# Optimization experiments

Hardware: AMD Instinct MI355X
Metric: run time of the kernel (lower is better)

## Reference

```python
import jax, jax.numpy as jnp
import numpy as np
import math

H, N2, RANK, CH, LMAX = 256, 64, 1, 1, 2048
DT_MIN, DT_MAX = 1e-3, 1e-1


def setup_inputs() -> dict:
    key = jax.random.key(0)
    kP, kPi, kC, kCi, kdt = jax.random.split(key, 5)
    # DPLR 'lin' init: A = -1/2 - i*pi*n  (real_part=0.5, imag_part=pi*arange(N//2))
    A_real = 0.5 * jnp.ones((H, N2), jnp.float32)
    A_imag = math.pi * jnp.broadcast_to(jnp.arange(N2, dtype=jnp.float32), (H, N2))
    # B_init='constant': B = ones (complex)
    B_real = jnp.ones((H, N2), jnp.float32)
    B_imag = jnp.zeros((H, N2), jnp.float32)
    # P = randn complex (rank, H, N//2); torch complex randn has per-component std 1/sqrt(2)
    s = 1.0 / math.sqrt(2.0)
    P_real = s * jax.random.normal(kP, (RANK, H, N2), jnp.float32)
    P_imag = s * jax.random.normal(kPi, (RANK, H, N2), jnp.float32)
    # C (output projection) randn complex (channels, H, N//2)
    C_real = s * jax.random.normal(kC, (CH, H, N2), jnp.float32)
    C_imag = s * jax.random.normal(kCi, (CH, H, N2), jnp.float32)
    # dt log-uniform in [dt_min, dt_max]
    log_dt = math.log(DT_MIN) + jax.random.uniform(kdt, (H,), jnp.float32) * (
        math.log(DT_MAX) - math.log(DT_MIN))
    return {
        "A_real": A_real, "A_imag": A_imag,
        "B_real": B_real, "B_imag": B_imag,
        "P_real": P_real, "P_imag": P_imag,
        "C_real": C_real, "C_imag": C_imag,
        "log_dt": log_dt, "L": LMAX,
    }


def _krylov_doubling(dA, dB, L):
    """Matrix-power doubling scan (mirrors `power`): columns [dB, dA dB, ..., dA^{L-1} dB].

    dA: (H, N, N) complex, dB: (H, N) complex -> (H, N, L) complex.
    """
    x = dB[..., None]  # (H, N, 1)
    Ap = dA
    while x.shape[-1] < L:
        x = jnp.concatenate([x, Ap @ x], axis=-1)  # doubling step
        Ap = Ap @ Ap  # repeated squaring, as in power()
    return x[..., :L]


def reference(A_real, A_imag, B_real, B_imag, P_real, P_imag, C_real, C_imag, log_dt, L):
    # Build DPLR state matrix: A = diag(Lambda) - P P^*
    Lam = (-A_real - 1j * A_imag).astype(jnp.complex64)        # (H, N2)
    P = (P_real + 1j * P_imag).astype(jnp.complex64)           # (R, H, N2)
    B = (B_real + 1j * B_imag).astype(jnp.complex64)           # (H, N2)
    C = (C_real + 1j * C_imag).astype(jnp.complex64)           # (CH, H, N2)
    n2 = Lam.shape[-1]
    I = jnp.eye(n2, dtype=jnp.complex64)
    A_mat = Lam[:, :, None] * I - jnp.einsum('rhn,rhm->hnm', P, jnp.conj(P))  # (H,N2,N2)
    dt = jnp.exp(log_dt).astype(jnp.complex64)                 # (H,)
    # Bilinear (Tustin) discretization: dA = (I - dt/2 A)^{-1}(I + dt/2 A), dB = (I - dt/2 A)^{-1} dt B
    half = 0.5 * dt[:, None, None] * A_mat
    M_bwd = I - half
    dA = jnp.linalg.solve(M_bwd, I + half)                     # (H,N2,N2)
    dB = jnp.linalg.solve(M_bwd, (dt[:, None] * B)[..., None])[..., 0]  # (H,N2)
    # Kernel via power-doubling Krylov scan, then project: K[c,h,l] = 2 Re(C dA^l dB)
    x = _krylov_doubling(dA, dB, L)                            # (H,N2,L)
    K = 2.0 * jnp.real(jnp.einsum('chn,hnl->chl', C, x))       # (CH,H,L)
    return K
```

## Files before the change

### kernel.cpp

```cpp
#include <hip/hip_runtime.h>


#define LL 2048

struct C2 { float re, im; };

__device__ __forceinline__ C2 cmul(C2 a, C2 b){ return {a.re*b.re - a.im*b.im, a.re*b.im + a.im*b.re}; }
__device__ __forceinline__ C2 cadd(C2 a, C2 b){ return {a.re+b.re, a.im+b.im}; }
__device__ __forceinline__ C2 csub(C2 a, C2 b){ return {a.re-b.re, a.im-b.im}; }
__device__ __forceinline__ C2 cinv(C2 a){ float s=1.0f/(a.re*a.re+a.im*a.im); return {a.re*s, -a.im*s}; }
__device__ __forceinline__ C2 cscale(float s, C2 a){ return {s*a.re, s*a.im}; }
__device__ __forceinline__ C2 ld2(float2 v){ return {v.x, v.y}; }
__device__ __forceinline__ float2 st2(C2 v){ return make_float2(v.re, v.im); }

template<int CTRL>
__device__ __forceinline__ float dpp_add(float x){
  int t = __builtin_amdgcn_update_dpp(0, __float_as_int(x), CTRL, 0xF, 0xF, true);
  return x + __int_as_float(t);
}
__device__ __forceinline__ float wave_sum63(float x){
  x = dpp_add<0xB1>(x);
  x = dpp_add<0x4E>(x);
  x = dpp_add<0x124>(x);
  x = dpp_add<0x128>(x);
  x = dpp_add<0x142>(x);
  x = dpp_add<0x143>(x);
  return x;
}
__device__ __forceinline__ float bcast63(float x){
  return __int_as_float(__builtin_amdgcn_readlane(__float_as_int(x), 63));
}
__device__ __forceinline__ float rdlane(float v, int l){
  return __int_as_float(__builtin_amdgcn_readlane(__float_as_int(v), l));
}
__device__ __forceinline__ float shr1(float x){
  return __int_as_float(__builtin_amdgcn_update_dpp(0, __float_as_int(x), 0x138, 0xF, 0xF, true));
}

__device__ __forceinline__ void tri_solve64(const C2 wl, C2 va, const int lane,
                                            float& so_re, float& so_im)
{
    C2 wsh = { shr1(wl.re), shr1(wl.im) };
    const float w0r = rdlane(wl.re, 0);
    const float w0i = rdlane(wl.im, 0);
    so_re = 0.0f; so_im = 0.0f;
    for (int j = 0; j < 64; j += 2) {
        const float s0r = rdlane(va.re, j);
        const float s0i = rdlane(va.im, j);
        const float v1r = rdlane(va.re, j + 1);
        const float v1i = rdlane(va.im, j + 1);
        const float s1r = v1r + (w0r*s0r - w0i*s0i);
        const float s1i = v1i + (w0r*s0i + w0i*s0r);
        if (lane == j)     { so_re = s0r; so_im = s0i; }
        if (lane == j + 1) { so_re = s1r; so_im = s1i; }
        const C2 wsh1 = { shr1(wsh.re), shr1(wsh.im) };
        va.re += wsh.re*s0r - wsh.im*s0i;
        va.im += wsh.re*s0i + wsh.im*s0r;
        va.re += wsh1.re*s1r - wsh1.im*s1i;
        va.im += wsh1.re*s1i + wsh1.im*s1r;
        wsh.re = shr1(wsh1.re);
        wsh.im = shr1(wsh1.im);
    }
}

__global__ __launch_bounds__(512)
__attribute__((amdgpu_waves_per_eu(2, 2)))
void ssm_dplr_kernel(
    const float* __restrict__ A_real, const float* __restrict__ A_imag,
    const float* __restrict__ B_real, const float* __restrict__ B_imag,
    const float* __restrict__ P_real, const float* __restrict__ P_imag,
    const float* __restrict__ C_real, const float* __restrict__ C_imag,
    const float* __restrict__ log_dt, float* __restrict__ out)
{
    const int h    = blockIdx.x;
    const int t    = threadIdx.x;
    const int lane = t & 63;
    const int wid  = t >> 6;

    extern __shared__ char sm[];
    float2* Abuf = (float2*)sm;
    float2* Cs   = (float2*)(sm + 32768);
    float2* tw   = Cs;
    float2* ta   = Cs + 512;
    float2* gA   = (float2*)(sm + 49152);
    float2* qA   = gA + 64;
    float2* g64A = gA + 128;
    float2* TgA  = gA + 192;
    float2* TpA  = gA + 256;
    float2* rqA  = gA + 320;
    float2* rxA  = gA + 384;
    float2* wvA  = gA + 448;
    float2* avA  = gA + 512;
    float2* cbuf = gA + 576;
    float2* prtC = gA + 640;
    int*    cntA = (int*)(gA + 1152);
    int*    flgA = cntA + 32;

    const int idx = h * 64 + lane;
    const float dt = expf(log_dt[h]);
    const float c  = 0.5f * dt;

    const C2 lam = { -A_real[idx], -A_imag[idx] };
    const C2 p   = {  P_real[idx],  P_imag[idx] };
    const C2 Bv  = {  B_real[idx],  B_imag[idx] };
    const C2 Cv  = {  C_real[idx],  C_imag[idx] };
    const C2 pc  = { p.re, -p.im };

    const C2 d = cinv(C2{ 1.0f - c*lam.re, -c*lam.im });
    const C2 g = cmul(d, C2{ 1.0f + c*lam.re, c*lam.im });

    C2 sv = cscale(p.re*p.re + p.im*p.im, d);
    C2 uv = cmul(cmul(d, pc), Bv);
    sv.re = bcast63(wave_sum63(sv.re)); sv.im = bcast63(wave_sum63(sv.im));
    uv.re = bcast63(wave_sum63(uv.re)); uv.im = bcast63(wave_sum63(uv.im));

    const C2 beta  = cscale(c, cinv(C2{ 1.0f + c*sv.re, c*sv.im }));
    const C2 bs    = cmul(beta, sv);
    const C2 gamma = { -c*(1.0f - bs.re), c*bs.im };

    const C2 q  = cmul(d, p);
    const C2 r  = cmul(pc, csub(gamma, cmul(beta, g)));
    const C2 x0 = cscale(dt, csub(cmul(d, Bv), cmul(cmul(beta, uv), q)));

    const C2 g2  = cmul(g,  g);
    const C2 g4  = cmul(g2, g2);
    const C2 g8  = cmul(g4, g4);
    const C2 g16 = cmul(g8, g8);
    const C2 g32 = cmul(g16,g16);
    const C2 g64 = cmul(g32,g32);

    if (wid == 0) {
        gA[lane]   = st2(g);
        qA[lane]   = st2(q);
        g64A[lane] = st2(g64);
        rqA[lane]  = st2(cmul(r, q));
        rxA[lane]  = st2(cmul(r, x0));
    }
    __syncthreads();

    {
        C2 cur = {1.0f, 0.0f};
        if (wid & 1) cur = g8;
        if (wid & 2) cur = cmul(cur, g16);
        if (wid & 4) cur = cmul(cur, g32);
        #pragma unroll
        for (int jj = 0; jj < 8; ++jj) {
            const int j = 8*wid + jj;
            Abuf[j*64 + ((lane + j) & 63)] = st2(cur);
            cur = cmul(cur, g);
        }
    }
    __syncthreads();

    {
        C2 accw = {0,0}, acca = {0,0};
        #pragma unroll
        for (int kk = 0; kk < 8; ++kk) {
            const int n = 8*wid + kk;
            const C2 Gv = ld2(Abuf[lane*64 + ((n + lane) & 63)]);
            const C2 fq = ld2(rqA[n]);
            const C2 fx = ld2(rxA[n]);
            accw = cadd(accw, cmul(Gv, fq));
            acca = cadd(acca, cmul(Gv, fx));
        }
        tw[wid*64 + lane] = st2(accw);
        ta[wid*64 + lane] = st2(acca);
    }
    __syncthreads();
    if (t < 64) {
        C2 sw = {0,0}, sa = {0,0};
        #pragma unroll
        for (int w2 = 0; w2 < 8; ++w2) {
            sw = cadd(sw, ld2(tw[w2*64 + t]));
            sa = cadd(sa, ld2(ta[w2*64 + t]));
        }
        wvA[t] = st2(sw);
        avA[t] = st2(sa);
    }
    __syncthreads();

    C2 idmk[8];
    #pragma unroll
    for (int kk = 0; kk < 8; ++kk) {
        idmk[kk] = cinv(csub(ld2(gA[8*wid + kk]), g));
    }
    if (wid == 0) {
        Cs[lane]   = st2(Cv);
        cbuf[lane] = st2(Cv);
        const C2 wl = ld2(wvA[lane]);
        float tau_re, tau_im;
        tri_solve64(wl, wl, lane, tau_re, tau_im);
        C2 pp = { rdlane(tau_re, 0), rdlane(tau_im, 0) };
        C2 dd = {0,0};
        for (int i = 1; i <= 62; ++i) {
            const C2 ti = { rdlane(tau_re, i), rdlane(tau_im, i) };
            dd = cadd(cmul(dd, g), pp);
            pp = cadd(cmul(pp, g), ti);
        }
        TgA[lane] = st2(cmul(g, pp));
        TpA[lane] = st2(cadd(pp, cmul(g, dd)));
    } else if (wid == 1) {
        const C2 wl = ld2(wvA[lane]);
        float sg_re, sg_im;
        tri_solve64(wl, ld2(avA[lane]), lane, sg_re, sg_im);
        C2 x = x0;
        for (int j = 0; j < 64; ++j) {
            Abuf[j*64 + ((lane + j) & 63)] = st2(x);
            const float sjr = rdlane(sg_re, j);
            const float sji = rdlane(sg_im, j);
            const float nr = g.re*x.re - g.im*x.im + sjr*q.re - sji*q.im;
            const float ni = g.re*x.im + g.im*x.re + sjr*q.im + sji*q.re;
            x.re = nr; x.im = ni;
        }
    } else if (wid == 2) {
        if (lane < 32)       cntA[lane] = 0;
        else                 flgA[lane - 32] = 0;
    }
    __syncthreads();

    C2 Mk[8];
    {
        const C2 Tgm = ld2(TgA[lane]);
        const C2 Tp  = ld2(TpA[lane]);
        const C2 g63 = cmul(g64, cinv(g));
        const C2 S   = cmul(r, cadd(cscale(64.0f, g63), Tp));
        const C2 diagv = cadd(g64, cmul(q, S));
        #pragma unroll
        for (int kk = 0; kk < 8; ++kk) {
            const int k = 8*wid + kk;
            const C2 qn   = ld2(qA[k]);
            const C2 g64n = ld2(g64A[k]);
            const C2 Tgn  = ld2(TgA[k]);
            const C2 num  = cmul(r, cadd(csub(g64n, g64), csub(Tgn, Tgm)));
            const C2 off  = cmul(cmul(qn, num), idmk[kk]);
            const bool isd = (lane == k);
            Mk[kk].re = isd ? diagv.re : off.re;
            Mk[kk].im = isd ? diagv.im : off.im;
        }
    }
    __syncthreads();

    {
        const float4* cb4 = (const float4*)cbuf;
        volatile int* vcnt = (volatile int*)cntA;
        volatile int* vflg = (volatile int*)flgA;
        for (int i = 1; i < 32; ++i) {
            if (i > 1) {
                while (vflg[i-1] == 0) { }
                __asm__ volatile("" ::: "memory");
            }
            const float4 ya = cb4[4*wid + 0];
            const float4 yb = cb4[4*wid + 1];
            const float4 yc = cb4[4*wid + 2];
            const float4 yd = cb4[4*wid + 3];
            float ar = 0.0f, ai = 0.0f;
            ar += ya.x*Mk[0].re - ya.y*Mk[0].im;  ai += ya.x*Mk[0].im + ya.y*Mk[0].re;
            ar += ya.z*Mk[1].re - ya.w*Mk[1].im;  ai += ya.z*Mk[1].im + ya.w*Mk[1].re;
            ar += yb.x*Mk[2].re - yb.y*Mk[2].im;  ai += yb.x*Mk[2].im + yb.y*Mk[2].re;
            ar += yb.z*Mk[3].re - yb.w*Mk[3].im;  ai += yb.z*Mk[3].im + yb.w*Mk[3].re;
            ar += yc.x*Mk[4].re - yc.y*Mk[4].im;  ai += yc.x*Mk[4].im + yc.y*Mk[4].re;
            ar += yc.z*Mk[5].re - yc.w*Mk[5].im;  ai += yc.z*Mk[5].im + yc.w*Mk[5].re;
            ar += yd.x*Mk[6].re - yd.y*Mk[6].im;  ai += yd.x*Mk[6].im + yd.y*Mk[6].re;
            ar += yd.z*Mk[7].re - yd.w*Mk[7].im;  ai += yd.z*Mk[7].im + yd.w*Mk[7].re;
            prtC[wid*64 + lane] = make_float2(ar, ai);
            __threadfence_block();
            if (lane == 0) atomicAdd(&cntA[i], 1);
            if (wid == 0) {
                while (vcnt[i] < 8) { }
                __asm__ volatile("" ::: "memory");
                C2 nc = {0,0};
                #pragma unroll
                for (int w2 = 0; w2 < 8; ++w2) {
                    const float2 pv = prtC[w2*64 + lane];
                    nc.re += pv.x; nc.im += pv.y;
                }
                cbuf[lane]      = st2(nc);
                Cs[i*64 + lane] = st2(nc);
                __threadfence_block();
                if (lane == 0) vflg[i] = 1;
            }
        }
    }
    __syncthreads();

    {
        float accK[4] = {0.0f, 0.0f, 0.0f, 0.0f};
        #pragma unroll 8
        for (int n = 0; n < 64; ++n) {
            const float2 xv = Abuf[lane*64 + ((n + lane) & 63)];
            #pragma unroll
            for (int rr = 0; rr < 4; ++rr) {
                const float2 cv = Cs[(4*wid + rr)*64 + n];
                accK[rr] += cv.x*xv.x - cv.y*xv.y;
            }
        }
        float* outh = out + h * LL;
        #pragma unroll
        for (int rr = 0; rr < 4; ++rr) {
            outh[(4*wid + rr)*64 + lane] = 2.0f * accK[rr];
        }
    }
}

extern "C" void kernel_launch(void* const* d_in, const int* in_sizes, int n_in,
                              void* d_out, int out_size, void* d_ws, size_t ws_size,
                              hipStream_t stream) {
    const float* A_real = (const float*)d_in[0];
    const float* A_imag = (const float*)d_in[1];
    const float* B_real = (const float*)d_in[2];
    const float* B_imag = (const float*)d_in[3];
    const float* P_real = (const float*)d_in[4];
    const float* P_imag = (const float*)d_in[5];
    const float* C_real = (const float*)d_in[6];
    const float* C_imag = (const float*)d_in[7];
    const float* log_dt = (const float*)d_in[8];
    float* out = (float*)d_out;

    const size_t lds = 49152 + 1152*sizeof(float2) + 256;
    ssm_dplr_kernel<<<256, 512, lds, stream>>>(
        A_real, A_imag, B_real, B_imag, P_real, P_imag,
        C_real, C_imag, log_dt, out);
}
```

Before: 101.9 us.

## Replace single-wave reduce plus flag handoff with redundant per-wave reductions

In the 31-step serial recurrence, every wave now reduces the eight partial products itself into its own private copy of the state vector, instead of waiting for wave 0 to reduce and publish a ready flag. The partial-product buffer is double-buffered by step parity so a fast wave cannot overwrite data still being read. This removes one spin-wait handoff and a serial reduction from each step's critical path, at the cost of eight times as many LDS reads per step. The shared-memory layout is reorganised so the per-wave buffers overlay the now-dead setup scratch.

```diff
diff --git a/kernel.cpp b/kernel.cpp
--- a/kernel.cpp
+++ b/kernel.cpp
@@ -87,14 +87,13 @@
     float2* g64A = gA + 128;
     float2* TgA  = gA + 192;
     float2* TpA  = gA + 256;
-    float2* rqA  = gA + 320;
-    float2* rxA  = gA + 384;
-    float2* wvA  = gA + 448;
-    float2* avA  = gA + 512;
-    float2* cbuf = gA + 576;
-    float2* prtC = gA + 640;
-    int*    cntA = (int*)(gA + 1152);
-    int*    flgA = cntA + 32;
+    float2* rqA  = (float2*)(sm + 51712);
+    float2* rxA  = rqA + 64;
+    float2* wvA  = rqA + 128;
+    float2* avA  = rqA + 192;
+    float2* cbufAll = (float2*)(sm + 51712);
+    float2* prtC    = (float2*)(sm + 55808);
+    int*    cntA    = (int*)(sm + 64000);
 
     const int idx = h * 64 + lane;
     const float dt = expf(log_dt[h]);
@@ -185,8 +184,7 @@
         idmk[kk] = cinv(csub(ld2(gA[8*wid + kk]), g));
     }
     if (wid == 0) {
-        Cs[lane]   = st2(Cv);
-        cbuf[lane] = st2(Cv);
+        Cs[lane] = st2(Cv);
         const C2 wl = ld2(wvA[lane]);
         float tau_re, tau_im;
         tri_solve64(wl, wl, lane, tau_re, tau_im);
@@ -213,8 +211,7 @@
             x.re = nr; x.im = ni;
         }
     } else if (wid == 2) {
-        if (lane < 32)       cntA[lane] = 0;
-        else                 flgA[lane - 32] = 0;
+        if (lane < 32) cntA[lane] = 0;
     }
     __syncthreads();
 
@@ -241,14 +238,12 @@
     __syncthreads();
 
     {
-        const float4* cb4 = (const float4*)cbuf;
+        float2* cb = cbufAll + wid*64;
+        const float4* cb4 = (const float4*)cb;
         volatile int* vcnt = (volatile int*)cntA;
-        volatile int* vflg = (volatile int*)flgA;
+        cb[lane] = st2(Cv);
         for (int i = 1; i < 32; ++i) {
-            if (i > 1) {
-                while (vflg[i-1] == 0) { }
-                __asm__ volatile("" ::: "memory");
-            }
+            const int buf = i & 1;
             const float4 ya = cb4[4*wid + 0];
             const float4 yb = cb4[4*wid + 1];
             const float4 yc = cb4[4*wid + 2];
@@ -262,23 +257,19 @@
             ar += yc.z*Mk[5].re - yc.w*Mk[5].im;  ai += yc.z*Mk[5].im + yc.w*Mk[5].re;
             ar += yd.x*Mk[6].re - yd.y*Mk[6].im;  ai += yd.x*Mk[6].im + yd.y*Mk[6].re;
             ar += yd.z*Mk[7].re - yd.w*Mk[7].im;  ai += yd.z*Mk[7].im + yd.w*Mk[7].re;
-            prtC[wid*64 + lane] = make_float2(ar, ai);
+            prtC[buf*512 + wid*64 + lane] = make_float2(ar, ai);
             __threadfence_block();
             if (lane == 0) atomicAdd(&cntA[i], 1);
-            if (wid == 0) {
-                while (vcnt[i] < 8) { }
-                __asm__ volatile("" ::: "memory");
-                C2 nc = {0,0};
-                #pragma unroll
-                for (int w2 = 0; w2 < 8; ++w2) {
-                    const float2 pv = prtC[w2*64 + lane];
-                    nc.re += pv.x; nc.im += pv.y;
-                }
-                cbuf[lane]      = st2(nc);
-                Cs[i*64 + lane] = st2(nc);
-                __threadfence_block();
-                if (lane == 0) vflg[i] = 1;
+            while (vcnt[i] < 8) { }
+            __asm__ volatile("" ::: "memory");
+            C2 nc = {0,0};
+            #pragma unroll
+            for (int w2 = 0; w2 < 8; ++w2) {
+                const float2 pv = prtC[buf*512 + w2*64 + lane];
+                nc.re += pv.x; nc.im += pv.y;
             }
+            cb[lane] = st2(nc);
+            if (wid == 0) Cs[i*64 + lane] = st2(nc);
         }
     }
     __syncthreads();
@@ -316,7 +307,7 @@
     const float* log_dt = (const float*)d_in[8];
     float* out = (float*)d_out;
 
-    const size_t lds = 49152 + 1152*sizeof(float2) + 256;
+    const size_t lds = 64128;
     ssm_dplr_kernel<<<256, 512, lds, stream>>>(
         A_real, A_imag, B_real, B_imag, P_real, P_imag,
         C_real, C_imag, log_dt, out);
```

Measured after the change: 101.8 us. About the same (-0.1%).
